# Kernel optimization log

Hardware: AMD Instinct MI355X
Metric: run time of the kernel (lower is better)

The kernel has to match this reference:

```python
import jax, jax.numpy as jnp
import numpy as np

N = 8192          # num_nodes
E = 262144        # num_edges = N * avg_degree(32)
K_SIGN = 1000.0   # ExactModel k
EPSILON = 5.0     # ExactModel epsilon


def setup_inputs() -> dict:
    key = jax.random.key(0)
    k1, k2, k3, k4 = jax.random.split(key, 4)
    src = jax.random.randint(k1, (E,), 0, N)
    dst = jax.random.randint(k2, (E,), 0, N)
    edge_index = jnp.stack([src, dst]).astype(jnp.int32)          # (2, E)
    # partition vector, elements in {1, ..., N}
    p = jax.random.randint(k3, (N,), 1, N + 1).astype(jnp.float32)  # (N,)
    x = jax.random.normal(k4, (N, 1), dtype=jnp.float32)            # node features
    return {"edge_index": edge_index, "p": p, "x": x}


def reference(edge_index, p, x):
    """infoco1 (segment logsumexp over edges with self-loops) followed by one
    refine step: pairwise difference matrix + CustomSignFunction tanh + row-sum."""
    n = p.shape[0]
    log_n = jnp.log(jnp.asarray(n, dtype=p.dtype))
    loops = jnp.arange(n, dtype=edge_index.dtype)
    src = jnp.concatenate([edge_index[0], loops])   # add_self_loops
    dst = jnp.concatenate([edge_index[1], loops])
    # contributions_log = log(p_i) + p_j * log(N)
    contrib = jnp.log(p[src]) + p[dst] * log_n      # (E + N,)
    # numerically stable segment log-sum-exp over incoming edges of each node
    mx = jax.ops.segment_max(contrib, dst, num_segments=n)              # scatter_max
    se = jax.ops.segment_sum(jnp.exp(contrib - mx[dst]), dst, num_segments=n)  # scatter_add
    S = mx + jnp.log(se) + jnp.dot(x[:, 0], p)      # infoco1: S_log + <x, p>
    # refine: all-pairs sign refinement, D_1 = tanh(k * (X - X^T) - eps)
    X = S[:, None]                                   # (N, 1)
    D1 = jnp.tanh(K_SIGN * (X - X.T) - EPSILON)      # (N, N)
    return D1.sum(axis=1)                            # (N,)
```

## Files before the change

kernel.cpp:

```cpp
#include <hip/hip_runtime.h>
#include <math.h>

#define K_SIGN 1000.0f
#define EPSILON 5.0f

#define D_HI ((EPSILON + 12.0f) / K_SIGN)
#define D_LO ((EPSILON - 12.0f) / K_SIGN)

#define NB_HIST 128


__global__ void __launch_bounds__(256) k_hist_aux(
        const int* __restrict__ src, const int* __restrict__ dst,
        const float* __restrict__ p, const float* __restrict__ x,
        int* __restrict__ Hpriv, double* __restrict__ C,
        int* __restrict__ PFX, int* __restrict__ order, int e, int n) {
    int tid = threadIdx.x;
    int b = blockIdx.x;
    if (b == NB_HIST) {
        __shared__ int hist[8192];
        __shared__ int pos[8192];
        __shared__ int csum[256];
        __shared__ double dred[4];
        int4* h4 = (int4*)hist;
        for (int i = tid; i < n / 4; i += 256) h4[i] = make_int4(0, 0, 0, 0);
        __syncthreads();
        for (int i = tid; i < n; i += 256)
            atomicAdd(&hist[(int)p[i] - 1], 1);
        __syncthreads();
        int cw = n / 256;
        int base = tid * cw;
        int s = 0;
        for (int k = 0; k < cw; ++k) s += hist[base + k];
        csum[tid] = s;
        __syncthreads();
        for (int off = 1; off < 256; off <<= 1) {
            int v = (tid >= off) ? csum[tid - off] : 0;
            __syncthreads();
            csum[tid] += v;
            __syncthreads();
        }
        int run = (tid == 0) ? 0 : csum[tid - 1];
        for (int k = 0; k < cw; ++k) {
            int h = hist[base + k];
            hist[base + k] = run;
            pos[base + k] = run;
            run += h;
        }
        __syncthreads();
        for (int i = tid; i < n; i += 256) {
            int r = atomicAdd(&pos[(int)p[i] - 1], 1);
            order[r] = i;
        }
        for (int k = tid; k < n; k += 256) PFX[k] = hist[k];
        if (tid == 0) PFX[n] = n;
        double acc = 0.0;
        for (int i = tid; i < n; i += 256)
            acc += (double)x[i] * (double)p[i];
        for (int off = 32; off > 0; off >>= 1)
            acc += __shfl_down(acc, off, 64);
        if ((tid & 63) == 0) dred[tid >> 6] = acc;
        __syncthreads();
        if (tid == 0) *C = dred[0] + dred[1] + dred[2] + dred[3];
        return;
    }
    __shared__ int th[8192];
    int4* t4 = (int4*)th;
    for (int i = tid; i < n / 4; i += 256) t4[i] = make_int4(0, 0, 0, 0);
    __syncthreads();
    int per = ((e + NB_HIST - 1) / NB_HIST + 3) & ~3;
    int t0 = b * per;
    int t1 = min(t0 + per, e);
    if (t0 < t1) {
        if ((((size_t)(src + t0) | (size_t)(dst + t0)) & 15) == 0) {
            int nv = (t1 - t0) & ~3;
            for (int t = t0 + tid * 4; t < t0 + nv; t += 1024) {
                int4 s4 = *(const int4*)(src + t);
                int4 d4 = *(const int4*)(dst + t);
                atomicAdd(&th[d4.x], (int)p[s4.x]);
                atomicAdd(&th[d4.y], (int)p[s4.y]);
                atomicAdd(&th[d4.z], (int)p[s4.z]);
                atomicAdd(&th[d4.w], (int)p[s4.w]);
            }
            for (int t = t0 + nv + tid; t < t1; t += 256)
                atomicAdd(&th[dst[t]], (int)p[src[t]]);
        } else {
            for (int t = t0 + tid; t < t1; t += 256)
                atomicAdd(&th[dst[t]], (int)p[src[t]]);
        }
    }
    __syncthreads();
    int4* o4 = (int4*)(Hpriv + b * n);
    for (int i = tid; i < n / 4; i += 256) o4[i] = t4[i];
}

__global__ void __launch_bounds__(256) k_merge(const int* __restrict__ Hpriv,
                                               const float* __restrict__ p,
                                               const double* __restrict__ C,
                                               float* __restrict__ S,
                                               int n, float log_n) {
    int i = blockIdx.x * 256 + threadIdx.x;
    if (i >= n) return;
    int t = (int)p[i];
#pragma unroll 8
    for (int b = 0; b < NB_HIST; ++b) t += Hpriv[b * n + i];
    S[i] = (logf((float)t) + p[i] * log_n) + (float)(*C);
}

__global__ void __launch_bounds__(256) k_out(const float* __restrict__ S,
                                             const float* __restrict__ p,
                                             const int* __restrict__ PFX,
                                             const int* __restrict__ order,
                                             float* __restrict__ out, int n) {
    int i = blockIdx.x * 256 + threadIdx.x;
    if (i >= n) return;
    int pi = (int)p[i];
    int base = PFX[pi - 1];
    int g = PFX[pi] - base;
    float si = S[i];
    float acc = (float)(base - (n - base - g));
    for (int k = 0; k < g; ++k) {
        int j = order[base + k];
        float d = si - S[j];
        if (d > D_HI) acc += 1.0f;
        else if (d < D_LO) acc -= 1.0f;
        else acc += tanhf(fmaf(K_SIGN, d, -EPSILON));
    }
    out[i] = acc;
}

extern "C" void kernel_launch(void* const* d_in, const int* in_sizes, int n_in,
                              void* d_out, int out_size, void* d_ws, size_t ws_size,
                              hipStream_t stream) {
    const int* edge_index = (const int*)d_in[0];
    const float* p = (const float*)d_in[1];
    const float* x = (const float*)d_in[2];
    float* out = (float*)d_out;

    int e = in_sizes[0] / 2;
    int n = in_sizes[1];
    const int* src = edge_index;
    const int* dst = edge_index + e;

    double* C = (double*)d_ws;
    float* S = (float*)((char*)d_ws + 16);
    int* PFX = (int*)(S + n);
    int* order = PFX + ((n + 1 + 3) & ~3);
    int* Hpriv = order + n;

    float log_n = logf((float)n);

    k_hist_aux<<<NB_HIST + 1, 256, 0, stream>>>(src, dst, p, x, Hpriv, C,
                                                PFX, order, e, n);
    k_merge<<<n / 256, 256, 0, stream>>>(Hpriv, p, C, S, n, log_n);
    k_out<<<n / 256, 256, 0, stream>>>(S, p, PFX, order, out, n);
}
```

Before: 106.4 us.

## Move order scatter into merge kernel, halve histogram blocks, drop vectorized edge loads

The aux block no longer builds the sorted order array. It only computes the bucket histogram, the prefix sums and the dot product, and the order scatter is moved into k_merge through a global pos array with atomics. The number of edge-histogram blocks drops from 128 to 64, which cuts the Hpriv partials that k_merge must read but doubles the edges each block processes. The int4-vectorized edge loads are replaced with scalar loads. The intent is to shorten the critical-path aux block, at the cost of less parallelism in the histogram phase and global atomics in merge.

Result: faster. 86.50 us (-18.7%).

```diff
diff --git a/kernel.cpp b/kernel.cpp
--- a/kernel.cpp
+++ b/kernel.cpp
@@ -7,104 +7,83 @@
 #define D_HI ((EPSILON + 12.0f) / K_SIGN)
 #define D_LO ((EPSILON - 12.0f) / K_SIGN)
 
-#define NB_HIST 128
+#define NB_HIST 64
 
 
-__global__ void __launch_bounds__(256) k_hist_aux(
+__global__ void __launch_bounds__(256) k_hist(
         const int* __restrict__ src, const int* __restrict__ dst,
         const float* __restrict__ p, const float* __restrict__ x,
         int* __restrict__ Hpriv, double* __restrict__ C,
-        int* __restrict__ PFX, int* __restrict__ order, int e, int n) {
+        int* __restrict__ PFX, int* __restrict__ pos, int e, int n) {
+    __shared__ int buf[8192];
+    __shared__ int csum[256];
+    __shared__ double dred[4];
     int tid = threadIdx.x;
     int b = blockIdx.x;
-    if (b == NB_HIST) {
-        __shared__ int hist[8192];
-        __shared__ int pos[8192];
-        __shared__ int csum[256];
-        __shared__ double dred[4];
-        int4* h4 = (int4*)hist;
-        for (int i = tid; i < n / 4; i += 256) h4[i] = make_int4(0, 0, 0, 0);
+
+    int4* b4 = (int4*)buf;
+    for (int i = tid; i < n / 4; i += 256) b4[i] = make_int4(0, 0, 0, 0);
+    __syncthreads();
+
+    if (b < NB_HIST) {
+        int per = (e + NB_HIST - 1) / NB_HIST;
+        int t0 = b * per;
+        int t1 = min(t0 + per, e);
+        for (int t = t0 + tid; t < t1; t += 256)
+            atomicAdd(&buf[dst[t]], (int)p[src[t]]);
         __syncthreads();
-        for (int i = tid; i < n; i += 256)
-            atomicAdd(&hist[(int)p[i] - 1], 1);
-        __syncthreads();
-        int cw = n / 256;
-        int base = tid * cw;
-        int s = 0;
-        for (int k = 0; k < cw; ++k) s += hist[base + k];
-        csum[tid] = s;
-        __syncthreads();
-        for (int off = 1; off < 256; off <<= 1) {
-            int v = (tid >= off) ? csum[tid - off] : 0;
-            __syncthreads();
-            csum[tid] += v;
-            __syncthreads();
-        }
-        int run = (tid == 0) ? 0 : csum[tid - 1];
-        for (int k = 0; k < cw; ++k) {
-            int h = hist[base + k];
-            hist[base + k] = run;
-            pos[base + k] = run;
-            run += h;
-        }
-        __syncthreads();
-        for (int i = tid; i < n; i += 256) {
-            int r = atomicAdd(&pos[(int)p[i] - 1], 1);
-            order[r] = i;
-        }
-        for (int k = tid; k < n; k += 256) PFX[k] = hist[k];
-        if (tid == 0) PFX[n] = n;
-        double acc = 0.0;
-        for (int i = tid; i < n; i += 256)
-            acc += (double)x[i] * (double)p[i];
-        for (int off = 32; off > 0; off >>= 1)
-            acc += __shfl_down(acc, off, 64);
-        if ((tid & 63) == 0) dred[tid >> 6] = acc;
-        __syncthreads();
-        if (tid == 0) *C = dred[0] + dred[1] + dred[2] + dred[3];
+        int4* o4 = (int4*)(Hpriv + b * n);
+        for (int i = tid; i < n / 4; i += 256) o4[i] = b4[i];
         return;
     }
-    __shared__ int th[8192];
-    int4* t4 = (int4*)th;
-    for (int i = tid; i < n / 4; i += 256) t4[i] = make_int4(0, 0, 0, 0);
+
+    double acc = 0.0;
+    for (int i = tid; i < n; i += 256) {
+        float pv = p[i];
+        atomicAdd(&buf[(int)pv - 1], 1);
+        acc += (double)x[i] * (double)pv;
+    }
+    for (int off = 32; off > 0; off >>= 1)
+        acc += __shfl_down(acc, off, 64);
+    if ((tid & 63) == 0) dred[tid >> 6] = acc;
     __syncthreads();
-    int per = ((e + NB_HIST - 1) / NB_HIST + 3) & ~3;
-    int t0 = b * per;
-    int t1 = min(t0 + per, e);
-    if (t0 < t1) {
-        if ((((size_t)(src + t0) | (size_t)(dst + t0)) & 15) == 0) {
-            int nv = (t1 - t0) & ~3;
-            for (int t = t0 + tid * 4; t < t0 + nv; t += 1024) {
-                int4 s4 = *(const int4*)(src + t);
-                int4 d4 = *(const int4*)(dst + t);
-                atomicAdd(&th[d4.x], (int)p[s4.x]);
-                atomicAdd(&th[d4.y], (int)p[s4.y]);
-                atomicAdd(&th[d4.z], (int)p[s4.z]);
-                atomicAdd(&th[d4.w], (int)p[s4.w]);
-            }
-            for (int t = t0 + nv + tid; t < t1; t += 256)
-                atomicAdd(&th[dst[t]], (int)p[src[t]]);
-        } else {
-            for (int t = t0 + tid; t < t1; t += 256)
-                atomicAdd(&th[dst[t]], (int)p[src[t]]);
-        }
+    if (tid == 0) *C = dred[0] + dred[1] + dred[2] + dred[3];
+
+    int cw = n / 256;
+    int base = tid * cw;
+    int s = 0;
+    for (int k = 0; k < cw; ++k) s += buf[base + k];
+    csum[tid] = s;
+    __syncthreads();
+    for (int off = 1; off < 256; off <<= 1) {
+        int v = (tid >= off) ? csum[tid - off] : 0;
+        __syncthreads();
+        csum[tid] += v;
+        __syncthreads();
     }
-    __syncthreads();
-    int4* o4 = (int4*)(Hpriv + b * n);
-    for (int i = tid; i < n / 4; i += 256) o4[i] = t4[i];
+    int run = (tid == 0) ? 0 : csum[tid - 1];
+    for (int k = 0; k < cw; ++k) {
+        int h = buf[base + k];
+        PFX[base + k] = run;
+        pos[base + k] = run;
+        run += h;
+    }
+    if (tid == 0) PFX[n] = n;
 }
 
-__global__ void __launch_bounds__(256) k_merge(const int* __restrict__ Hpriv,
-                                               const float* __restrict__ p,
-                                               const double* __restrict__ C,
-                                               float* __restrict__ S,
-                                               int n, float log_n) {
+__global__ void __launch_bounds__(256) k_merge(
+        const int* __restrict__ Hpriv, const float* __restrict__ p,
+        const double* __restrict__ C, float* __restrict__ S,
+        int* __restrict__ pos, int* __restrict__ order, int n, float log_n) {
     int i = blockIdx.x * 256 + threadIdx.x;
     if (i >= n) return;
-    int t = (int)p[i];
+    float pv = p[i];
+    int t = (int)pv;
 #pragma unroll 8
     for (int b = 0; b < NB_HIST; ++b) t += Hpriv[b * n + i];
-    S[i] = (logf((float)t) + p[i] * log_n) + (float)(*C);
+    S[i] = (logf((float)t) + pv * log_n) + (float)(*C);
+    int r = atomicAdd(&pos[(int)pv - 1], 1);
+    order[r] = i;
 }
 
 __global__ void __launch_bounds__(256) k_out(const float* __restrict__ S,
@@ -145,13 +124,14 @@
     double* C = (double*)d_ws;
     float* S = (float*)((char*)d_ws + 16);
     int* PFX = (int*)(S + n);
-    int* order = PFX + ((n + 1 + 3) & ~3);
+    int* pos = PFX + (n + 4);
+    int* order = pos + n;
     int* Hpriv = order + n;
 
     float log_n = logf((float)n);
 
-    k_hist_aux<<<NB_HIST + 1, 256, 0, stream>>>(src, dst, p, x, Hpriv, C,
-                                                PFX, order, e, n);
-    k_merge<<<n / 256, 256, 0, stream>>>(Hpriv, p, C, S, n, log_n);
+    k_hist<<<NB_HIST + 1, 256, 0, stream>>>(src, dst, p, x, Hpriv, C,
+                                            PFX, pos, e, n);
+    k_merge<<<n / 256, 256, 0, stream>>>(Hpriv, p, C, S, pos, order, n, log_n);
     k_out<<<n / 256, 256, 0, stream>>>(S, p, PFX, order, out, n);
 }
```
